# Performance work log

Hardware: AMD Instinct MI355X
Metric: run time of the kernel (lower is better)

Reference implementation:

```python
import jax, jax.numpy as jnp
import numpy as np

B, S, D_MODEL = 2, 8192, 768
NUM_HEADS = 12
R = 4          # dilation_rate (= number of independent attention branches)
SEG = 512      # segment_size


def setup_inputs() -> dict:
    key = jax.random.key(0)
    ks = jax.random.split(key, 3)
    x = jax.random.normal(ks[0], (B, S, D_MODEL), jnp.float32)
    # Per-offset MHA weights: fused qkv proj and output proj (bias zeros)
    Wqkv = jax.random.normal(ks[1], (R, 3 * D_MODEL, D_MODEL), jnp.float32) * 0.02
    bqkv = jnp.zeros((R, 3 * D_MODEL), jnp.float32)
    Wout = jax.random.normal(ks[2], (R, D_MODEL, D_MODEL), jnp.float32) * 0.02
    bout = jnp.zeros((R, D_MODEL), jnp.float32)
    return {"x": x, "Wqkv": Wqkv, "bqkv": bqkv, "Wout": Wout, "bout": bout,
            "num_heads": NUM_HEADS}


def reference(x, Wqkv, bqkv, Wout, bout, num_heads):
    Bb, Ss, D = x.shape
    r = Wqkv.shape[0]
    L = Ss // r                # tokens per dilation offset
    n_seg = L // SEG           # segments per offset
    hd = D // num_heads

    # Dilated strided gather: x[:, o::r, :] for all offsets o -> (r, B, L, D)
    xo = jnp.moveaxis(x.reshape(Bb, L, r, D), 2, 0)

    # Per-offset fused qkv projection
    qkv = jnp.einsum('rbld,red->rble', xo, Wqkv) + bqkv[:, None, None, :]
    q, k, v = jnp.split(qkv, 3, axis=-1)
    seg = lambda t: t.reshape(r, Bb, n_seg, SEG, num_heads, hd)
    q, k, v = seg(q), seg(k), seg(v)  # (r, B, n_seg, SEG, H, hd)

    scale = 1.0 / np.sqrt(hd).astype(np.float32)
    scores = jnp.einsum('rbnqhd,rbnkhd->rbnhqk', q, k) * scale
    attn = jax.nn.softmax(scores, axis=-1)
    ctx = jnp.einsum('rbnhqk,rbnkhd->rbnqhd', attn, v).reshape(r, Bb, L, D)

    # Per-offset output projection
    out = jnp.einsum('rbld,red->rble', ctx, Wout) + bout[:, None, None, :]  # (r,B,L,D)

    # Scatter each offset's output back to its strided positions, zeros elsewhere,
    # then concat over offsets along the feature dim -> (B, S, r*D)
    res = jnp.zeros((Bb, Ss, r * D), x.dtype)
    for o in range(r):  # fixed small loop over dilation offsets
        res = res.at[:, o::r, o * D:(o + 1) * D].set(out[o])
    return res
```

## Files before the change

kernel.cpp:

```cpp
#include <hip/hip_runtime.h>

constexpr int Bb   = 2;
constexpr int S    = 8192;
constexpr int D    = 768;
constexpr int H    = 12;
constexpr int HD   = 64;
constexpr int R    = 4;
constexpr int L    = 2048;
constexpr int SEG  = 512;
constexpr int NSEG = 4;
constexpr int E3   = 3 * D;
constexpr int RD   = R * D;

typedef _Float16 f16x8 __attribute__((ext_vector_type(8)));
typedef _Float16 f16x4 __attribute__((ext_vector_type(4)));
typedef float    f32x4 __attribute__((ext_vector_type(4)));

#define AS1 __attribute__((address_space(1)))
#define AS3 __attribute__((address_space(3)))

__device__ __forceinline__ void gld16(const void* g, void* l) {
    __builtin_amdgcn_global_load_lds((AS1 void*)g, (AS3 void*)l, 16, 0, 0);
}

__global__ __launch_bounds__(256) void zero_fill(float4* __restrict__ p, int n4)
{
    int i = blockIdx.x * 256 + threadIdx.x;
    const int stride = gridDim.x * 256;
    float4 z; z.x = z.y = z.z = z.w = 0.f;
    for (; i < n4; i += stride) p[i] = z;
}

__global__ __launch_bounds__(256) void conv_split(const float4* __restrict__ x,
                                                  f16x4* __restrict__ hi,
                                                  f16x4* __restrict__ lo, int n4)
{
    int i = blockIdx.x * 256 + threadIdx.x;
    const int stride = gridDim.x * 256;
    for (; i < n4; i += stride) {
        float4 v = x[i];
        f16x4 h, l;
        h[0] = (_Float16)v.x; l[0] = (_Float16)(v.x - (float)h[0]);
        h[1] = (_Float16)v.y; l[1] = (_Float16)(v.y - (float)h[1]);
        h[2] = (_Float16)v.z; l[2] = (_Float16)(v.z - (float)h[2]);
        h[3] = (_Float16)v.w; l[3] = (_Float16)(v.w - (float)h[3]);
        hi[i] = h; lo[i] = l;
    }
}

__global__ __launch_bounds__(256) void conv_one(const float4* __restrict__ x,
                                                f16x4* __restrict__ o, int n4)
{
    int i = blockIdx.x * 256 + threadIdx.x;
    const int stride = gridDim.x * 256;
    for (; i < n4; i += stride) {
        float4 v = x[i];
        f16x4 h;
        h[0] = (_Float16)v.x; h[1] = (_Float16)v.y;
        h[2] = (_Float16)v.z; h[3] = (_Float16)v.w;
        o[i] = h;
    }
}

template <int MODE>
__global__ __launch_bounds__(256) void mfma_gemm(const _Float16* __restrict__ Ah0,
                                                 const _Float16* __restrict__ Wh0,
                                                 const _Float16* __restrict__ Wl0,
                                                 const float* __restrict__ B0,
                                                 _Float16* __restrict__ Q0,
                                                 _Float16* __restrict__ K0,
                                                 _Float16* __restrict__ V0,
                                                 float* __restrict__ C0)
{
    const int z = blockIdx.z;
    const int r = z >> 1, b = z & 1;

    const _Float16* Ah; const _Float16* Wh; const _Float16* Wl = nullptr;
    const float* bias;
    int lda;
    if (MODE == 0) {
        Ah = Ah0 + ((size_t)b * S + r) * D;  lda = RD;
        Wh = Wh0 + (size_t)r * E3 * D;
        Wl = Wl0 + (size_t)r * E3 * D;
        bias = B0 + r * E3;
    } else {
        Ah = Ah0 + (size_t)z * L * D;        lda = D;
        Wh = Wh0 + (size_t)r * D * D;
        bias = B0 + r * D;
    }

    const int tid  = threadIdx.x;
    const int wave = tid >> 6;
    const int lane = tid & 63;
    const int lw   = lane & 15;
    const int quad = lane >> 4;
    const int wm   = wave & 1, wn = wave >> 1;
    const int m0 = blockIdx.y * 128, n0 = blockIdx.x * 128;

    constexpr int NTILE = (MODE == 0) ? 3 : 2;
    __shared__ _Float16 sm[NTILE * 4096];
    constexpr int TAH = 0;
    constexpr int TWH = 4096;
    constexpr int TWL = 8192;

    f32x4 acc[4][4];
    #pragma unroll
    for (int mt = 0; mt < 4; mt++)
        #pragma unroll
        for (int nt = 0; nt < 4; nt++)
            acc[mt][nt] = f32x4{0.f, 0.f, 0.f, 0.f};

    const int srow = lane & 15;
    const int scol = (lane >> 4) * 8;

    for (int k0 = 0; k0 < 768; k0 += 32) {
        __syncthreads();
        if (MODE == 0) {
            #pragma unroll
            for (int i = 0; i < 6; i++) {
                const int idx  = wave * 6 + i;
                const int tile = idx >> 3, g = idx & 7;
                const _Float16* src = (tile == 0) ? Ah : (tile == 1) ? Wh : Wl;
                const int ldr   = (tile == 0) ? lda : D;
                const int base0 = (tile == 0) ? m0 : n0;
                gld16(src + (size_t)(base0 + g * 16 + srow) * ldr + k0 + scol,
                      &sm[tile * 4096 + g * 512]);
            }
        } else {
            #pragma unroll
            for (int i = 0; i < 4; i++) {
                const int idx  = wave * 4 + i;
                const int tile = idx >> 3, g = idx & 7;
                const _Float16* src = (tile == 0) ? Ah : Wh;
                const int ldr   = (tile == 0) ? lda : D;
                const int base0 = (tile == 0) ? m0 : n0;
                gld16(src + (size_t)(base0 + g * 16 + srow) * ldr + k0 + scol,
                      &sm[tile * 4096 + g * 512]);
            }
        }
        __syncthreads();

        f16x8 afh[4], bfh[4];
        #pragma unroll
        for (int mt = 0; mt < 4; mt++)
            afh[mt] = *(const f16x8*)&sm[TAH + (wm * 4 + mt) * 512 + quad * 128 + lw * 8];
        #pragma unroll
        for (int nt = 0; nt < 4; nt++)
            bfh[nt] = *(const f16x8*)&sm[TWH + (wn * 4 + nt) * 512 + quad * 128 + lw * 8];
        #pragma unroll
        for (int mt = 0; mt < 4; mt++)
            #pragma unroll
            for (int nt = 0; nt < 4; nt++)
                acc[mt][nt] = __builtin_amdgcn_mfma_f32_16x16x32_f16(afh[mt], bfh[nt], acc[mt][nt], 0, 0, 0);

        if (MODE == 0) {
            f16x8 bfl[4];
            #pragma unroll
            for (int nt = 0; nt < 4; nt++)
                bfl[nt] = *(const f16x8*)&sm[TWL + (wn * 4 + nt) * 512 + quad * 128 + lw * 8];
            #pragma unroll
            for (int mt = 0; mt < 4; mt++)
                #pragma unroll
                for (int nt = 0; nt < 4; nt++)
                    acc[mt][nt] = __builtin_amdgcn_mfma_f32_16x16x32_f16(afh[mt], bfl[nt], acc[mt][nt], 0, 0, 0);
        }
    }
    __syncthreads();

    float bv[4];
    #pragma unroll
    for (int nt = 0; nt < 4; nt++)
        bv[nt] = bias[n0 + wn * 64 + nt * 16 + lw];

    if (MODE == 0) {
        const int reg = n0 / D;
        if (reg < 2) {
            _Float16* G = (reg == 0 ? Q0 : K0) + (size_t)z * L * D;
            const int colbase = (n0 - reg * D) + wn * 64;
            _Float16* wbuf = &sm[wave * 2048];
            #pragma unroll
            for (int p = 0; p < 2; p++) {
                #pragma unroll
                for (int mtl = 0; mtl < 2; mtl++) {
                    const int mt = p * 2 + mtl;
                    #pragma unroll
                    for (int nt = 0; nt < 4; nt++)
                        #pragma unroll
                        for (int rr = 0; rr < 4; rr++)
                            wbuf[(mtl * 16 + quad * 4 + rr) * 64 + nt * 16 + lw] =
                                (_Float16)(acc[mt][nt][rr] + bv[nt]);
                }
                asm volatile("s_waitcnt lgkmcnt(0)" ::: "memory");
                #pragma unroll
                for (int j = 0; j < 4; j++) {
                    const int rl = (lane >> 3) + j * 8;
                    f16x8 v = *(const f16x8*)&wbuf[rl * 64 + (lane & 7) * 8];
                    const int l = m0 + wm * 64 + p * 32 + rl;
                    *(f16x8*)(G + (size_t)l * D + colbase + (lane & 7) * 8) = v;
                }
                asm volatile("s_waitcnt lgkmcnt(0)" ::: "memory");
            }
        } else {
            #pragma unroll
            for (int nt = 0; nt < 4; nt++) {
                const int e  = (n0 - 2 * D) + wn * 64 + nt * 16 + lw;
                const int hh = e >> 6, hd = e & 63;
                #pragma unroll
                for (int mt = 0; mt < 4; mt++) {
                    const int l = m0 + wm * 64 + mt * 16 + quad * 4;
                    const int ns = l >> 9, key = l & 511;
                    f16x4 v;
                    #pragma unroll
                    for (int rr = 0; rr < 4; rr++)
                        v[rr] = (_Float16)(acc[mt][nt][rr] + bv[nt]);
                    *(f16x4*)(V0 + ((size_t)((z * H + hh) * NSEG + ns)) * (HD * SEG)
                              + (size_t)hd * SEG + key) = v;
                }
            }
        }
    } else {
        float* Cb = C0 + (size_t)b * S * RD + r * RD + r * D;
        #pragma unroll
        for (int mt = 0; mt < 4; mt++)
            #pragma unroll
            for (int nt = 0; nt < 4; nt++) {
                const int col = n0 + wn * 64 + nt * 16 + lw;
                #pragma unroll
                for (int rr = 0; rr < 4; rr++)
                    Cb[(size_t)(m0 + wm * 64 + mt * 16 + quad * 4 + rr) * (R * RD) + col] =
                        acc[mt][nt][rr] + bv[nt];
            }
    }
}

__global__ __launch_bounds__(256) void attn_mfma(const _Float16* __restrict__ Qh,
                                                 const _Float16* __restrict__ Kh,
                                                 const _Float16* __restrict__ Vt,
                                                 _Float16* __restrict__ ctx)
{
    __shared__ _Float16 Ks[4096];
    __shared__ _Float16 Vs[4096];
    __shared__ _Float16 Pw[16384];

    int t = blockIdx.x;
    const int qh = t & 1; t >>= 1;
    const int h  = t % H; t /= H;
    const int n  = t & 3; t >>= 2;
    const int z  = t;

    const int tid  = threadIdx.x;
    const int wave = tid >> 6;
    const int lane = tid & 63;
    const int lw   = lane & 15;
    const int quad = lane >> 4;
    const int srow = lane & 15;
    const int scol = (lane >> 4) * 8;

    const _Float16* Qg = Qh + ((size_t)(z * L + n * SEG + qh * 256)) * D + h * HD;
    #pragma unroll
    for (int i = 0; i < 8; i++) {
        const int qg = wave * 4 + (i >> 1), h2 = i & 1;
        gld16(Qg + (size_t)(qg * 16 + srow) * D + h2 * 32 + scol,
              &Pw[qg * 1024 + h2 * 512]);
    }
    __syncthreads();

    f16x8 qf[4][2];
    #pragma unroll
    for (int mt = 0; mt < 4; mt++)
        #pragma unroll
        for (int kk = 0; kk < 2; kk++)
            qf[mt][kk] = *(const f16x8*)&Pw[(wave * 4 + mt) * 1024 + (kk * 4 + quad) * 128 + lw * 8];

    const _Float16* Kg = Kh + ((size_t)(z * L + n * SEG)) * D + h * HD;
    const _Float16* Vg = Vt + ((size_t)((z * H + h) * NSEG + n)) * (HD * SEG);
    _Float16* Pv = Pw + wave * 4096;

    f32x4 cacc[4][4];
    #pragma unroll
    for (int mt = 0; mt < 4; mt++)
        #pragma unroll
        for (int nt = 0; nt < 4; nt++)
            cacc[mt][nt] = f32x4{0.f, 0.f, 0.f, 0.f};
    float psum[4] = {0.f, 0.f, 0.f, 0.f};

    for (int kt = 0; kt < 8; kt++) {
        __syncthreads();
        #pragma unroll
        for (int i = 0; i < 4; i++) {
            const int idx = wave * 4 + i;
            const int j = idx & 7, g = j >> 1, h2 = j & 1;
            if (idx < 8)
                gld16(Kg + (size_t)(kt * 64 + g * 16 + srow) * D + h2 * 32 + scol,
                      &Ks[g * 1024 + h2 * 512]);
            else
                gld16(Vg + (size_t)(g * 16 + srow) * SEG + kt * 64 + h2 * 32 + scol,
                      &Vs[g * 1024 + h2 * 512]);
        }
        __syncthreads();

        f32x4 Sc[4][4];
        #pragma unroll
        for (int mt = 0; mt < 4; mt++)
            #pragma unroll
            for (int nt = 0; nt < 4; nt++)
                Sc[mt][nt] = f32x4{0.f, 0.f, 0.f, 0.f};
        #pragma unroll
        for (int kk = 0; kk < 2; kk++)
            #pragma unroll
            for (int nt = 0; nt < 4; nt++) {
                f16x8 kf = *(const f16x8*)&Ks[nt * 1024 + (kk * 4 + quad) * 128 + lw * 8];
                #pragma unroll
                for (int mt = 0; mt < 4; mt++)
                    Sc[mt][nt] = __builtin_amdgcn_mfma_f32_16x16x32_f16(kf, qf[mt][kk], Sc[mt][nt], 0, 0, 0);
            }

        #pragma unroll
        for (int mt = 0; mt < 4; mt++)
            #pragma unroll
            for (int nt = 0; nt < 4; nt++) {
                f16x4 p4;
                #pragma unroll
                for (int rr = 0; rr < 4; rr++)
                    p4[rr] = (_Float16)__expf(Sc[mt][nt][rr] * 0.125f);
                *(f16x4*)&Pv[mt * 1024 + (nt * 2 + (quad >> 1)) * 128 + lw * 8 + (quad & 1) * 4] = p4;
            }
        asm volatile("s_waitcnt lgkmcnt(0)" ::: "memory");

        #pragma unroll
        for (int kk = 0; kk < 2; kk++) {
            f16x8 pf[4], vf[4];
            #pragma unroll
            for (int mt = 0; mt < 4; mt++) {
                pf[mt] = *(const f16x8*)&Pv[mt * 1024 + (kk * 4 + quad) * 128 + lw * 8];
                float s = 0.f;
                #pragma unroll
                for (int j = 0; j < 8; j++) s += (float)pf[mt][j];
                psum[mt] += s;
            }
            #pragma unroll
            for (int nt = 0; nt < 4; nt++)
                vf[nt] = *(const f16x8*)&Vs[nt * 1024 + (kk * 4 + quad) * 128 + lw * 8];
            #pragma unroll
            for (int mt = 0; mt < 4; mt++)
                #pragma unroll
                for (int nt = 0; nt < 4; nt++)
                    cacc[mt][nt] = __builtin_amdgcn_mfma_f32_16x16x32_f16(pf[mt], vf[nt], cacc[mt][nt], 0, 0, 0);
        }
    }

    #pragma unroll
    for (int mt = 0; mt < 4; mt++) {
        psum[mt] += __shfl_xor(psum[mt], 16);
        psum[mt] += __shfl_xor(psum[mt], 32);
    }
    _Float16* Cg = ctx + ((size_t)(z * L + n * SEG + qh * 256 + wave * 64)) * D + h * HD;
    #pragma unroll
    for (int mt = 0; mt < 4; mt++)
        #pragma unroll
        for (int rr = 0; rr < 4; rr++) {
            float iv = 1.0f / __shfl(psum[mt], quad * 4 + rr);
            int q = mt * 16 + quad * 4 + rr;
            #pragma unroll
            for (int nt = 0; nt < 4; nt++)
                Cg[(size_t)q * D + nt * 16 + lw] = (_Float16)(cacc[mt][nt][rr] * iv);
        }
}

extern "C" void kernel_launch(void* const* d_in, const int* in_sizes, int n_in,
                              void* d_out, int out_size, void* d_ws, size_t ws_size,
                              hipStream_t stream)
{
    const float* x    = (const float*)d_in[0];
    const float* Wqkv = (const float*)d_in[1];
    const float* bqkv = (const float*)d_in[2];
    const float* Wout = (const float*)d_in[3];
    const float* bout = (const float*)d_in[4];

    float* out = (float*)d_out;

    constexpr size_t NX   = (size_t)Bb * S * D;
    constexpr size_t NWQ  = (size_t)R * E3 * D;
    constexpr size_t NWO  = (size_t)R * D * D;
    constexpr size_t NTOK = (size_t)R * Bb * L;

    _Float16* Xh  = (_Float16*)d_ws;
    _Float16* Wqh = Xh  + NX;
    _Float16* Wql = Wqh + NWQ;
    _Float16* Wo  = Wql + NWQ;
    _Float16* Qh  = Wo  + NWO;
    _Float16* Kh  = Qh  + NTOK * D;
    _Float16* Vt  = Kh  + NTOK * D;
    _Float16* ctx = Vt  + NTOK * D;

    zero_fill<<<2048, 256, 0, stream>>>((float4*)out, (Bb * S * RD) / 4);

    conv_one<<<2048, 256, 0, stream>>>((const float4*)x, (f16x4*)Xh, (int)(NX / 4));
    conv_split<<<2048, 256, 0, stream>>>((const float4*)Wqkv, (f16x4*)Wqh, (f16x4*)Wql, (int)(NWQ / 4));
    conv_one<<<1024, 256, 0, stream>>>((const float4*)Wout, (f16x4*)Wo, (int)(NWO / 4));

    mfma_gemm<0><<<dim3(E3 / 128, L / 128, R * Bb), 256, 0, stream>>>(
        Xh, Wqh, Wql, bqkv, Qh, Kh, Vt, nullptr);

    attn_mfma<<<R * Bb * NSEG * H * 2, 256, 0, stream>>>(Qh, Kh, Vt, ctx);

    mfma_gemm<1><<<dim3(D / 128, L / 128, R * Bb), 256, 0, stream>>>(
        ctx, Wo, nullptr, bout, nullptr, nullptr, nullptr, out);
}
```

Baseline: 551.6 us.

## Drop split-fp16 Wqkv correction and double-buffer GEMM LDS loads

Removes the hi/lo fp16 split of the QKV weights, so the QKV GEMM does one MFMA pass instead of two and the conv_split kernel becomes a plain conversion. The GEMM main loop also gains double-buffered LDS staging: the next K-slice is prefetched with global_load_lds while the current one is consumed, and the barriers per iteration drop from two to one. This cuts MFMA work, weight-conversion traffic and load latency stalls, at the cost of lower accuracy in the QKV projection, which may affect the tolerance check.

New measurement: 487.4 us. -11.6%, faster.

```diff
diff --git a/kernel.cpp b/kernel.cpp
--- a/kernel.cpp
+++ b/kernel.cpp
@@ -31,23 +31,6 @@
     for (; i < n4; i += stride) p[i] = z;
 }
 
-__global__ __launch_bounds__(256) void conv_split(const float4* __restrict__ x,
-                                                  f16x4* __restrict__ hi,
-                                                  f16x4* __restrict__ lo, int n4)
-{
-    int i = blockIdx.x * 256 + threadIdx.x;
-    const int stride = gridDim.x * 256;
-    for (; i < n4; i += stride) {
-        float4 v = x[i];
-        f16x4 h, l;
-        h[0] = (_Float16)v.x; l[0] = (_Float16)(v.x - (float)h[0]);
-        h[1] = (_Float16)v.y; l[1] = (_Float16)(v.y - (float)h[1]);
-        h[2] = (_Float16)v.z; l[2] = (_Float16)(v.z - (float)h[2]);
-        h[3] = (_Float16)v.w; l[3] = (_Float16)(v.w - (float)h[3]);
-        hi[i] = h; lo[i] = l;
-    }
-}
-
 __global__ __launch_bounds__(256) void conv_one(const float4* __restrict__ x,
                                                 f16x4* __restrict__ o, int n4)
 {
@@ -65,7 +48,6 @@
 template <int MODE>
 __global__ __launch_bounds__(256) void mfma_gemm(const _Float16* __restrict__ Ah0,
                                                  const _Float16* __restrict__ Wh0,
-                                                 const _Float16* __restrict__ Wl0,
                                                  const float* __restrict__ B0,
                                                  _Float16* __restrict__ Q0,
                                                  _Float16* __restrict__ K0,
@@ -75,13 +57,11 @@
     const int z = blockIdx.z;
     const int r = z >> 1, b = z & 1;
 
-    const _Float16* Ah; const _Float16* Wh; const _Float16* Wl = nullptr;
-    const float* bias;
+    const _Float16* Ah; const _Float16* Wh; const float* bias;
     int lda;
     if (MODE == 0) {
         Ah = Ah0 + ((size_t)b * S + r) * D;  lda = RD;
         Wh = Wh0 + (size_t)r * E3 * D;
-        Wl = Wl0 + (size_t)r * E3 * D;
         bias = B0 + r * E3;
     } else {
         Ah = Ah0 + (size_t)z * L * D;        lda = D;
@@ -97,11 +77,7 @@
     const int wm   = wave & 1, wn = wave >> 1;
     const int m0 = blockIdx.y * 128, n0 = blockIdx.x * 128;
 
-    constexpr int NTILE = (MODE == 0) ? 3 : 2;
-    __shared__ _Float16 sm[NTILE * 4096];
-    constexpr int TAH = 0;
-    constexpr int TWH = 4096;
-    constexpr int TWL = 8192;
+    __shared__ _Float16 sm[2][2][4096];
 
     f32x4 acc[4][4];
     #pragma unroll
@@ -113,57 +89,37 @@
     const int srow = lane & 15;
     const int scol = (lane >> 4) * 8;
 
-    for (int k0 = 0; k0 < 768; k0 += 32) {
+    auto stage = [&](int buf, int k0) {
+        #pragma unroll
+        for (int i = 0; i < 4; i++) {
+            const int idx  = wave * 4 + i;
+            const int tile = idx >> 3, g = idx & 7;
+            const _Float16* src = (tile == 0) ? Ah : Wh;
+            const int ldr   = (tile == 0) ? lda : D;
+            const int base0 = (tile == 0) ? m0 : n0;
+            gld16(src + (size_t)(base0 + g * 16 + srow) * ldr + k0 + scol,
+                  &sm[buf][tile][g * 512]);
+        }
+    };
+
+    stage(0, 0);
+
+    for (int k = 0; k < 24; k++) {
         __syncthreads();
-        if (MODE == 0) {
-            #pragma unroll
-            for (int i = 0; i < 6; i++) {
-                const int idx  = wave * 6 + i;
-                const int tile = idx >> 3, g = idx & 7;
-                const _Float16* src = (tile == 0) ? Ah : (tile == 1) ? Wh : Wl;
-                const int ldr   = (tile == 0) ? lda : D;
-                const int base0 = (tile == 0) ? m0 : n0;
-                gld16(src + (size_t)(base0 + g * 16 + srow) * ldr + k0 + scol,
-                      &sm[tile * 4096 + g * 512]);
-            }
-        } else {
-            #pragma unroll
-            for (int i = 0; i < 4; i++) {
-                const int idx  = wave * 4 + i;
-                const int tile = idx >> 3, g = idx & 7;
-                const _Float16* src = (tile == 0) ? Ah : Wh;
-                const int ldr   = (tile == 0) ? lda : D;
-                const int base0 = (tile == 0) ? m0 : n0;
-                gld16(src + (size_t)(base0 + g * 16 + srow) * ldr + k0 + scol,
-                      &sm[tile * 4096 + g * 512]);
-            }
-        }
-        __syncthreads();
-
-        f16x8 afh[4], bfh[4];
-        #pragma unroll
-        for (int mt = 0; mt < 4; mt++)
-            afh[mt] = *(const f16x8*)&sm[TAH + (wm * 4 + mt) * 512 + quad * 128 + lw * 8];
+        const int buf = k & 1;
+        f16x8 af[4], bf[4];
+        #pragma unroll
+        for (int mt = 0; mt < 4; mt++)
+            af[mt] = *(const f16x8*)&sm[buf][0][(wm * 4 + mt) * 512 + quad * 128 + lw * 8];
         #pragma unroll
         for (int nt = 0; nt < 4; nt++)
-            bfh[nt] = *(const f16x8*)&sm[TWH + (wn * 4 + nt) * 512 + quad * 128 + lw * 8];
+            bf[nt] = *(const f16x8*)&sm[buf][1][(wn * 4 + nt) * 512 + quad * 128 + lw * 8];
+        if (k + 1 < 24) stage(buf ^ 1, (k + 1) * 32);
         #pragma unroll
         for (int mt = 0; mt < 4; mt++)
             #pragma unroll
             for (int nt = 0; nt < 4; nt++)
-                acc[mt][nt] = __builtin_amdgcn_mfma_f32_16x16x32_f16(afh[mt], bfh[nt], acc[mt][nt], 0, 0, 0);
-
-        if (MODE == 0) {
-            f16x8 bfl[4];
-            #pragma unroll
-            for (int nt = 0; nt < 4; nt++)
-                bfl[nt] = *(const f16x8*)&sm[TWL + (wn * 4 + nt) * 512 + quad * 128 + lw * 8];
-            #pragma unroll
-            for (int mt = 0; mt < 4; mt++)
-                #pragma unroll
-                for (int nt = 0; nt < 4; nt++)
-                    acc[mt][nt] = __builtin_amdgcn_mfma_f32_16x16x32_f16(afh[mt], bfl[nt], acc[mt][nt], 0, 0, 0);
-        }
+                acc[mt][nt] = __builtin_amdgcn_mfma_f32_16x16x32_f16(af[mt], bf[nt], acc[mt][nt], 0, 0, 0);
     }
     __syncthreads();
 
@@ -177,7 +133,7 @@
         if (reg < 2) {
             _Float16* G = (reg == 0 ? Q0 : K0) + (size_t)z * L * D;
             const int colbase = (n0 - reg * D) + wn * 64;
-            _Float16* wbuf = &sm[wave * 2048];
+            _Float16* wbuf = &sm[0][0][wave * 2048];
             #pragma unroll
             for (int p = 0; p < 2; p++) {
                 #pragma unroll
@@ -386,8 +342,7 @@
 
     _Float16* Xh  = (_Float16*)d_ws;
     _Float16* Wqh = Xh  + NX;
-    _Float16* Wql = Wqh + NWQ;
-    _Float16* Wo  = Wql + NWQ;
+    _Float16* Wo  = Wqh + NWQ;
     _Float16* Qh  = Wo  + NWO;
     _Float16* Kh  = Qh  + NTOK * D;
     _Float16* Vt  = Kh  + NTOK * D;
@@ -396,14 +351,14 @@
     zero_fill<<<2048, 256, 0, stream>>>((float4*)out, (Bb * S * RD) / 4);
 
     conv_one<<<2048, 256, 0, stream>>>((const float4*)x, (f16x4*)Xh, (int)(NX / 4));
-    conv_split<<<2048, 256, 0, stream>>>((const float4*)Wqkv, (f16x4*)Wqh, (f16x4*)Wql, (int)(NWQ / 4));
+    conv_one<<<2048, 256, 0, stream>>>((const float4*)Wqkv, (f16x4*)Wqh, (int)(NWQ / 4));
     conv_one<<<1024, 256, 0, stream>>>((const float4*)Wout, (f16x4*)Wo, (int)(NWO / 4));
 
     mfma_gemm<0><<<dim3(E3 / 128, L / 128, R * Bb), 256, 0, stream>>>(
-        Xh, Wqh, Wql, bqkv, Qh, Kh, Vt, nullptr);
+        Xh, Wqh, bqkv, Qh, Kh, Vt, nullptr);
 
     attn_mfma<<<R * Bb * NSEG * H * 2, 256, 0, stream>>>(Qh, Kh, Vt, ctx);
 
     mfma_gemm<1><<<dim3(D / 128, L / 128, R * Bb), 256, 0, stream>>>(
-        ctx, Wo, nullptr, bout, nullptr, nullptr, nullptr, out);
-}
+        ctx, Wo, bout, nullptr, nullptr, nullptr, out);
+}
```
